# Optimization experiments

Measured on AMD Instinct MI355X. Metric: run time of the kernel, lower is better.

The kernel has to match this reference:

```python
import jax, jax.numpy as jnp
import numpy as np

MASK = 1
PAD = 0
N_ITER = 3
B, N, D, VOCAB = 8, 1024, 256, 32000
PAD_START = 960  # positions >= PAD_START are PAD tokens


def make_positional(d, max_len):
    pos = jnp.arange(max_len, dtype=jnp.float32)[:, None]          # [L,1]
    di = jnp.arange(d // 2, dtype=jnp.float32) / (d // 2)          # [d/2]
    ang = (10000.0 ** (-di))[None, :] * pos                        # [L,d/2]
    return jnp.concatenate([jnp.sin(ang), jnp.cos(ang)], axis=-1)  # [L,d]


def setup_inputs() -> dict:
    rng = np.random.default_rng(0)
    ix = rng.integers(2, VOCAB, size=(B, N), dtype=np.int64)
    ix[:, PAD_START:] = PAD
    pos = np.arange(PAD_START)
    mpos = pos[pos % 15 == 7]                      # 64 masked positions per row
    ix[:, mpos] = MASK
    mask_idx = (np.arange(B)[:, None] * N + mpos[None, :]).reshape(-1).astype(np.int32)  # [512]

    key = jax.random.key(0)
    k1, k2, k3, k4 = jax.random.split(key, 4)
    emb = jax.random.normal(k1, (VOCAB, D), dtype=jnp.float32) * 0.02
    Wq = jax.random.normal(k2, (D, D), dtype=jnp.float32) * 0.02
    Wk = jax.random.normal(k3, (D, D), dtype=jnp.float32) * 0.02
    Wv = jax.random.normal(k4, (D, D), dtype=jnp.float32) * 0.02
    return {"ix": jnp.asarray(ix), "mask_idx": jnp.asarray(mask_idx),
            "emb": emb, "Wq": Wq, "Wk": Wk, "Wv": Wv}


def reference(ix, mask_idx, emb, Wq, Wk, Wv):
    d = emb.shape[1]
    n = ix.shape[-1]
    sqd = np.sqrt(d).astype(np.float32)
    PE = make_positional(d, n)                                  # [n,d]

    mask = (ix == MASK)[..., None]                              # [B,n,1] bool
    pad = (ix == PAD)[..., None].astype(jnp.float32)            # [B,n,1]
    padm = (pad + jnp.swapaxes(pad, -2, -1)) > 0                # [B,n,n] bool
    mask_inf = jnp.where(padm, -9999.0, 0.0).astype(jnp.float32)

    X = jnp.where(mask, 0.0, emb[ix])                           # [B,n,d]
    Q = jnp.zeros((X.shape[0], n, d), jnp.float32)
    K = jnp.zeros_like(Q)
    V = jnp.zeros_like(Q)
    H = jnp.zeros_like(Q)
    S = jnp.zeros((X.shape[0], n, n), jnp.float32)

    def update_S(Q, K, H, V):
        scores = (jnp.einsum('bnd,bmd->bnm', Q, K)
                  + jnp.einsum('bnd,bmd->bnm', H, V) + mask_inf) / sqd
        Sn = jax.nn.softmax(scores, axis=-1)
        return jnp.where(padm, 0.0, Sn)

    logits = None
    for _ in range(N_ITER):
        Xp = X + PE[None]                                       # [B,n,d]
        Q = Xp @ Wq.T + S @ K
        K = Xp @ Wk.T + jnp.einsum('bmn,bmd->bnd', S, Q)        # S^T @ Q
        V = Xp @ Wv.T + jnp.einsum('bmn,bmd->bnd', S, H)        # S^T @ H
        S = update_S(Q, K, H, V)
        H = S @ V
        S = update_S(Q, K, H, V)
        V = Xp @ Wv.T + jnp.einsum('bmn,bmd->bnd', S, H)
        K = Xp @ Wk.T + jnp.einsum('bmn,bmd->bnd', S, Q)
        Q = Xp @ Wq.T + S @ K
        Xm = V @ Wv + K @ Wk + Q @ Wq                           # [B,n,d] (note: no transpose, as in torch)
        X = jnp.where(mask, Xm, X)
        Xm_rows = Xm.reshape(-1, d)[mask_idx]                   # [n_masked, d]
        logits = Xm_rows @ emb.T                                # [n_masked, vocab]
    return logits
```

## Files before the change

### kernel.cpp

```cpp
#include <hip/hip_runtime.h>
#include <hip/hip_bf16.h>
#include <hip/hip_fp16.h>

typedef __attribute__((ext_vector_type(8))) short bf16x8;
typedef __attribute__((ext_vector_type(4))) float f32x4;
typedef unsigned short u16;

static __device__ __forceinline__ u16 f2bf(float f) {
    union { float f; unsigned int i; } c; c.f = f;
    unsigned int r = c.i + 0x7fffu + ((c.i >> 16) & 1u);
    return (u16)(r >> 16);
}
static __device__ __forceinline__ u16 f2h(float f) {
    __half h = __float2half(f);
    return *(u16*)&h;
}
static __device__ __forceinline__ float h2f(u16 u) {
    __half h = *(__half*)&u;
    return __half2float(h);
}

#define AS1(p) ((const __attribute__((address_space(1))) void*)(p))
#define AS3(p) ((__attribute__((address_space(3))) void*)(p))
static __device__ __forceinline__ void glds16(const void* g, void* l) {
    __builtin_amdgcn_global_load_lds(AS1(g), AS3(l), 16, 0, 0);
}

static __device__ __forceinline__ void xcdmap(int nwg, int nx, int& x, int& y, int& z) {
    const int lin = blockIdx.x;
    const int per = nwg >> 3;
    const int swz = (lin & 7) * per + (lin >> 3);
    z = swz / per;
    const int rem = swz - z * per;
    x = rem % nx;
    y = rem / nx;
}

static constexpr long B_EMB  = 0;
static constexpr long B_SF   = 16777216;
static constexpr long B_SXP  = B_SF   + 33554432;
static constexpr long B_STXP = B_SXP  + 20971520;
static constexpr long B_QH   = B_STXP + 20971520;
static constexpr long B_KVQ  = B_QH   + 8388608;
static constexpr long B_BQ   = B_KVQ  + 12582912;
static constexpr long B_BKV  = B_BQ   + 5242880;
static constexpr long B_VT   = B_BKV  + 10485760;
static constexpr long B_W3T  = B_VT   + 4194304;
static constexpr long B_XRB  = B_W3T  + 393216;
static constexpr long B_PE   = B_XRB  + 262144;
static constexpr long B_PAD  = B_PE   + 1048576;
static constexpr long B_MSK  = B_PAD  + 32768;

static constexpr long sSX  = 1024L * 1280;
static constexpr long sQH  = 1024L * 512;
static constexpr long sKVQ = 1024L * 768;
static constexpr long sBQ  = 256L * 1280;
static constexpr long sBKV = 512L * 1280;
static constexpr long sVT  = 256L * 1024;
static constexpr long sS2  = 1024L * 1024;

__global__ __launch_bounds__(256) void k_setup(float* __restrict__ PE, const int* __restrict__ ix,
                                               int* __restrict__ padf, int* __restrict__ maskf,
                                               const float* __restrict__ Wq, const float* __restrict__ Wk,
                                               const float* __restrict__ Wv, const float* __restrict__ emb,
                                               char* __restrict__ base) {
    __shared__ u16 tile[32][33];
    const int bid = blockIdx.x;
    if (bid < 512) {
        int g = bid * 256 + threadIdx.x;
        int p = g >> 7, j = g & 127;
        float di   = (float)j * (1.0f / 128.0f);
        float freq = powf(10000.0f, -di);
        float ang  = (float)p * freq;
        PE[(long)p * 256 + j]       = sinf(ang);
        PE[(long)p * 256 + j + 128] = cosf(ang);
        return;
    }
    if (bid < 544) {
        int g = (bid - 512) * 256 + threadIdx.x;
        int tok = ix[g];
        padf[g]  = (tok == 0) ? 1 : 0;
        maskf[g] = (tok == 1) ? 1 : 0;
        return;
    }
    if (bid < 2080) {
        const int idx = bid - 544;
        const int bz = idx >> 6, rem = idx & 63;
        const int bx = rem >> 3, by = rem & 7;
        const int ws = bz >> 3, rb8 = bz & 7;
        const float* W; u16 *rep, *T; long repStride;
        if (ws == 0)      { W = Wk; rep = (u16*)(base + B_BKV);               T = (u16*)(base + B_W3T);       repStride = sBKV; }
        else if (ws == 1) { W = Wv; rep = (u16*)(base + B_BKV) + 256L * 1280; T = (u16*)(base + B_W3T) + 256; repStride = sBKV; }
        else              { W = Wq; rep = (u16*)(base + B_BQ);                T = (u16*)(base + B_W3T) + 512; repStride = sBQ; }
        rep += (long)rb8 * repStride;
        const int tx = threadIdx.x & 31, ty = threadIdx.x >> 5;
#pragma unroll
        for (int rr = 0; rr < 32; rr += 8) {
            int r = bx * 32 + ty + rr, c = by * 32 + tx;
            u16 u = f2bf(W[(long)r * 256 + c]);
            rep[(long)r * 1280 + c] = u;
            if (rb8 == 0) tile[ty + rr][tx] = u;
        }
        if (rb8 == 0) {
            __syncthreads();
#pragma unroll
            for (int rr = 0; rr < 32; rr += 8)
                T[(long)(by * 32 + ty + rr) * 768 + bx * 32 + tx] = tile[tx][ty + rr];
        }
        return;
    }
    long e = ((long)(bid - 2080) * 256 + threadIdx.x) * 4;
    float4 v = *(const float4*)(emb + e);
    ushort4 o;
    o.x = f2bf(v.x); o.y = f2bf(v.y); o.z = f2bf(v.z); o.w = f2bf(v.w);
    *(ushort4*)((u16*)(base + B_EMB) + e) = o;
}

__global__ __launch_bounds__(256) void k_embx(const int* __restrict__ ix, const float* __restrict__ emb,
                                              const float* __restrict__ PE,
                                              u16* __restrict__ SXp, u16* __restrict__ STXp) {
    int g = blockIdx.x * 256 + threadIdx.x;
    long e = (long)g * 4;
    long bn = e >> 8;
    int i = (int)(bn & 1023), c = (int)(e & 255);
    int tok = ix[bn];
    float4 v;
    if (tok == 1) v = make_float4(0.f, 0.f, 0.f, 0.f);
    else          v = *(const float4*)(emb + (long)tok * 256 + c);
    float4 p = *(const float4*)(PE + (long)i * 256 + c);
    ushort4 o;
    o.x = f2bf(v.x + p.x); o.y = f2bf(v.y + p.y);
    o.z = f2bf(v.z + p.z); o.w = f2bf(v.w + p.w);
    long oo = bn * 1280 + c;
    *(ushort4*)(SXp + oo)  = o;
    *(ushort4*)(STXp + oo) = o;
}

__global__ __launch_bounds__(256)
void k_gupd(const u16* __restrict__ SXp, const u16* __restrict__ STXp,
            u16* __restrict__ BQ, u16* __restrict__ BKV,
            u16* __restrict__ QHb, u16* __restrict__ KVQ, u16* __restrict__ VTb, int K) {
    int xb, y, z;
    xcdmap(768, 8, xb, y, z);
    const int i0 = xb * 128;
    const u16 *A, *B;
    u16 *outR, *outR2, *T;
    int j0, ldR, ldT, jloc;
    if (y < 4) {
        j0 = y << 6;
        A = SXp + (long)z * sSX;  B = BQ + (long)z * sBQ;
        outR  = QHb + (long)z * sQH;          ldR = 512;
        outR2 = KVQ + 512 + (long)z * sKVQ;
        T = BKV + 256 + (long)z * sBKV;       ldT = 1280; jloc = j0;
    } else {
        j0 = (y - 4) << 6;
        A = STXp + (long)z * sSX;  B = BKV + (long)z * sBKV;
        outR  = KVQ + (long)z * sKVQ;         ldR = 768;
        outR2 = nullptr;
        if (j0 < 256) { T = BQ + 256 + (long)z * sBQ; ldT = 1280; jloc = j0; }
        else          { T = VTb + (long)z * sVT;      ldT = 1024; jloc = j0 - 256; }
    }

    __shared__ u16 As[128 * 32];
    __shared__ u16 Bs[64 * 32];
    __shared__ u16 Tt[64][136];
    const int t = threadIdx.x, w = t >> 6, l = t & 63;
    const int wr = (w >> 1) << 6, wc = (w & 1) << 5;
    const int lr = l & 15, lk = (l >> 4) << 3;
    f32x4 acc[4][2] = {};

    const u16* ga = A + (long)(i0 + (t >> 2)) * 1280 + ((t & 3) << 3);
    const u16* gb = B + (long)(j0 + (t >> 2)) * 1280 + ((t & 3) << 3);
    const long a64 = 1280L << 6;
    char* lA = (char*)As + (w << 10);
    char* lB = (char*)Bs + (w << 10);

    for (int k0 = 0; k0 < K; k0 += 32) {
        glds16(ga + k0,       lA);
        glds16(ga + k0 + a64, lA + 4096);
        glds16(gb + k0,       lB);
        __syncthreads();
        bf16x8 af[4], bb[2];
#pragma unroll
        for (int m = 0; m < 4; ++m)
            af[m] = *(const bf16x8*)(As + ((wr + (m << 4) + lr) << 5) + lk);
#pragma unroll
        for (int n = 0; n < 2; ++n)
            bb[n] = *(const bf16x8*)(Bs + ((wc + (n << 4) + lr) << 5) + lk);
#pragma unroll
        for (int m = 0; m < 4; ++m)
#pragma unroll
            for (int n = 0; n < 2; ++n)
                acc[m][n] = __builtin_amdgcn_mfma_f32_16x16x32_bf16(af[m], bb[n], acc[m][n], 0, 0, 0);
        __syncthreads();
    }

    const int rb  = wr + ((l >> 4) << 2);
    const int cbl = wc + lr;
#pragma unroll
    for (int m = 0; m < 4; ++m)
#pragma unroll
        for (int n = 0; n < 2; ++n)
#pragma unroll
            for (int j = 0; j < 4; ++j) {
                u16 u = f2bf(acc[m][n][j]);
                int rl = rb + (m << 4) + j;
                int cl = cbl + (n << 4);
                outR[(long)(i0 + rl) * ldR + j0 + cl] = u;
                if (outR2) outR2[(long)(i0 + rl) * 768 + j0 + cl] = u;
                Tt[cl][rl] = u;
            }
    __syncthreads();
#pragma unroll
    for (int p = 0; p < 4; ++p) {
        int id = p * 256 + t;
        int jj = id >> 4, ch = id & 15;
        uint4 v = *(const uint4*)&Tt[jj][ch << 3];
        *(uint4*)(T + (long)(jloc + jj) * ldT + i0 + (ch << 3)) = v;
    }
}

__global__ __launch_bounds__(256)
void k_gbf(int nwg, int ny,
           const u16* __restrict__ A, int lda, long sA, int K,
           const u16* __restrict__ B, int ldb, long sB,
           u16* __restrict__ outR, int ldR, long sR,
           u16* __restrict__ outR2, int ldR2, long sR2,
           u16* __restrict__ outT1, int ldT1, long sT1,
           u16* __restrict__ outT2, int ldT2, long sT2, int jSplit) {
    int xb, yb, z;
    xcdmap(nwg, 8, xb, yb, z);
    (void)ny;
    A    += (long)z * sA;
    B    += (long)z * sB;
    outR += (long)z * sR;
    if (outR2) outR2 += (long)z * sR2;
    const int i0 = xb * 128, j0 = yb * 64;
    u16* T; int ldT; long sT; int jloc;
    if (j0 < jSplit) { T = outT1; ldT = ldT1; sT = sT1; jloc = j0; }
    else             { T = outT2; ldT = ldT2; sT = sT2; jloc = j0 - jSplit; }
    T += (long)z * sT;

    __shared__ u16 As[128 * 32];
    __shared__ u16 Bs[64 * 32];
    __shared__ u16 Tt[64][136];
    const int t = threadIdx.x, w = t >> 6, l = t & 63;
    const int wr = (w >> 1) << 6, wc = (w & 1) << 5;
    const int lr = l & 15, lk = (l >> 4) << 3;
    f32x4 acc[4][2] = {};

    const u16* ga = A + (long)(i0 + (t >> 2)) * lda + ((t & 3) << 3);
    const u16* gb = B + (long)(j0 + (t >> 2)) * ldb + ((t & 3) << 3);
    const long a64 = (long)lda << 6;
    char* lA = (char*)As + (w << 10);
    char* lB = (char*)Bs + (w << 10);

    for (int k0 = 0; k0 < K; k0 += 32) {
        glds16(ga + k0,       lA);
        glds16(ga + k0 + a64, lA + 4096);
        glds16(gb + k0,       lB);
        __syncthreads();
        bf16x8 af[4], bb[2];
#pragma unroll
        for (int m = 0; m < 4; ++m)
            af[m] = *(const bf16x8*)(As + ((wr + (m << 4) + lr) << 5) + lk);
#pragma unroll
        for (int n = 0; n < 2; ++n)
            bb[n] = *(const bf16x8*)(Bs + ((wc + (n << 4) + lr) << 5) + lk);
#pragma unroll
        for (int m = 0; m < 4; ++m)
#pragma unroll
            for (int n = 0; n < 2; ++n)
                acc[m][n] = __builtin_amdgcn_mfma_f32_16x16x32_bf16(af[m], bb[n], acc[m][n], 0, 0, 0);
        __syncthreads();
    }

    const int rb  = wr + ((l >> 4) << 2);
    const int cbl = wc + lr;
#pragma unroll
    for (int m = 0; m < 4; ++m)
#pragma unroll
        for (int n = 0; n < 2; ++n)
#pragma unroll
            for (int j = 0; j < 4; ++j) {
                u16 u = f2bf(acc[m][n][j]);
                int rl = rb + (m << 4) + j;
                int cl = cbl + (n << 4);
                outR[(long)(i0 + rl) * ldR + j0 + cl] = u;
                if (outR2) outR2[(long)(i0 + rl) * ldR2 + j0 + cl] = u;
                Tt[cl][rl] = u;
            }
    __syncthreads();
#pragma unroll
    for (int p = 0; p < 4; ++p) {
        int id = p * 256 + t;
        int jj = id >> 4, ch = id & 15;
        uint4 v = *(const uint4*)&Tt[jj][ch << 3];
        *(uint4*)(T + (long)(jloc + jj) * ldT + i0 + (ch << 3)) = v;
    }
}

__global__ __launch_bounds__(256)
void k_mf(const u16* __restrict__ A, const u16* __restrict__ B, u16* __restrict__ C,
          int K, int lda, int ldb, int ldc, long sA, long sB, long sC) {
    int xb, yb, z;
    xcdmap(512, 8, xb, yb, z);
    A += (long)z * sA;
    B += (long)z * sB;
    C += (long)z * sC;
    const int i0 = xb * 128, j0 = yb * 128;
    __shared__ u16 As[128 * 32];
    __shared__ u16 Bs[128 * 32];
    const int t = threadIdx.x, w = t >> 6, l = t & 63;
    const int wr = (w >> 1) << 6, wc = (w & 1) << 6;
    const int lr = l & 15, lk = (l >> 4) << 3;
    f32x4 acc[4][4] = {};
    const u16* ga = A + (long)(i0 + (t >> 2)) * lda + ((t & 3) << 3);
    const u16* gb = B + (long)(j0 + (t >> 2)) * ldb + ((t & 3) << 3);
    const long a64 = (long)lda << 6, b64 = (long)ldb << 6;
    char* lA = (char*)As + (w << 10);
    char* lB = (char*)Bs + (w << 10);
    for (int k0 = 0; k0 < K; k0 += 32) {
        glds16(ga + k0,       lA);
        glds16(ga + k0 + a64, lA + 4096);
        glds16(gb + k0,       lB);
        glds16(gb + k0 + b64, lB + 4096);
        __syncthreads();
        bf16x8 af[4], bfr[4];
#pragma unroll
        for (int m = 0; m < 4; ++m)
            af[m] = *(const bf16x8*)(As + ((wr + (m << 4) + lr) << 5) + lk);
#pragma unroll
        for (int n = 0; n < 4; ++n)
            bfr[n] = *(const bf16x8*)(Bs + ((wc + (n << 4) + lr) << 5) + lk);
#pragma unroll
        for (int m = 0; m < 4; ++m)
#pragma unroll
            for (int n = 0; n < 4; ++n)
                acc[m][n] = __builtin_amdgcn_mfma_f32_16x16x32_bf16(af[m], bfr[n], acc[m][n], 0, 0, 0);
        __syncthreads();
    }
    const int rb = i0 + wr + ((l >> 4) << 2);
    const int cb = j0 + wc + lr;
#pragma unroll
    for (int m = 0; m < 4; ++m)
#pragma unroll
        for (int n = 0; n < 4; ++n)
#pragma unroll
            for (int j = 0; j < 4; ++j)
                C[(long)(rb + (m << 4) + j) * ldc + cb + (n << 4)] = f2h(acc[m][n][j]);
}

__global__ __launch_bounds__(256)
void k_smtr(const u16* __restrict__ Sf, u16* __restrict__ SXp, u16* __restrict__ STXp,
            const int* __restrict__ padf) {
    int bx, yb, b;
    xcdmap(1024, 128, bx, yb, b);
    (void)yb;
    const int t = threadIdx.x;
    const int r = t >> 5, cg = t & 31;
    __shared__ u16   T8[8][1028];
    __shared__ float padd[1024];
    const int r0 = bx * 8;
    const int row = r0 + r;
    const int* pr = padf + b * 1024;
#pragma unroll
    for (int k = 0; k < 4; ++k)
        padd[t * 4 + k] = pr[t * 4 + k] ? -9999.0f : 0.0f;
    __syncthreads();
    const float prow = pr[row] ? -9999.0f : 0.0f;
    const u16* src = Sf + ((long)(b * 1024 + row)) * 1024;

    float e[32];
    float m = -3.0e38f;
#pragma unroll
    for (int q = 0; q < 8; ++q) {
        int c = cg * 4 + q * 128;
        ushort4 v = *(const ushort4*)(src + c);
#pragma unroll
        for (int j = 0; j < 4; ++j) {
            float x = (h2f((&v.x)[j]) + fminf(prow, padd[c + j])) * 0.0625f;
            e[q * 4 + j] = x;
            m = fmaxf(m, x);
        }
    }
#pragma unroll
    for (int o = 1; o < 32; o <<= 1) m = fmaxf(m, __shfl_xor(m, o));

    float s = 0.f;
#pragma unroll
    for (int i = 0; i < 32; ++i) { e[i] = expf(e[i] - m); s += e[i]; }
#pragma unroll
    for (int o = 1; o < 32; o <<= 1) s += __shfl_xor(s, o);
    const float inv = 1.0f / s;

    u16* orow = SXp + ((long)(b * 1024 + row)) * 1280 + 256;
#pragma unroll
    for (int q = 0; q < 8; ++q) {
        int c = cg * 4 + q * 128;
        ushort4 o4;
#pragma unroll
        for (int j = 0; j < 4; ++j)
            (&o4.x)[j] = (fminf(prow, padd[c + j]) < 0.f) ? (u16)0 : f2bf(e[q * 4 + j] * inv);
        *(ushort4*)(orow + c) = o4;
        *(ushort4*)&T8[r][c] = o4;
    }
    __syncthreads();
#pragma unroll
    for (int p = 0; p < 4; ++p) {
        int c = t + p * 256;
        u16 tmp[8];
#pragma unroll
        for (int rr = 0; rr < 8; ++rr) tmp[rr] = T8[rr][c];
        *(uint4*)(STXp + ((long)(b * 1024 + c)) * 1280 + 256 + r0) = *(uint4*)&tmp[0];
    }
}

__global__ __launch_bounds__(256)
void k_xmr(const u16* __restrict__ KVQ, const u16* __restrict__ W3T,
           const int* __restrict__ midx, const float* __restrict__ PE,
           u16* __restrict__ SXp, u16* __restrict__ STXp, u16* __restrict__ XRb, int last) {
    const int i0 = blockIdx.x * 128, j0 = blockIdx.y * 64;
    __shared__ u16 As[128 * 32];
    __shared__ u16 Bs[64 * 32];
    const int t = threadIdx.x, w = t >> 6, l = t & 63;
    const int wr = (w >> 1) << 6, wc = (w & 1) << 5;
    const int lr = l & 15, lk = (l >> 4) << 3;
    f32x4 acc[4][2] = {};
    const int r1 = i0 + (t >> 2);
    const u16* ga1 = KVQ + (long)midx[r1]      * 768 + ((t & 3) << 3);
    const u16* ga2 = KVQ + (long)midx[r1 + 64] * 768 + ((t & 3) << 3);
    const u16* gb  = W3T + (long)(j0 + (t >> 2)) * 768 + ((t & 3) << 3);
    char* lA = (char*)As + (w << 10);
    char* lB = (char*)Bs + (w << 10);
    for (int k0 = 0; k0 < 768; k0 += 32) {
        glds16(ga1 + k0, lA);
        glds16(ga2 + k0, lA + 4096);
        glds16(gb  + k0, lB);
        __syncthreads();
        bf16x8 af[4], bb[2];
#pragma unroll
        for (int m = 0; m < 4; ++m)
            af[m] = *(const bf16x8*)(As + ((wr + (m << 4) + lr) << 5) + lk);
#pragma unroll
        for (int n = 0; n < 2; ++n)
            bb[n] = *(const bf16x8*)(Bs + ((wc + (n << 4) + lr) << 5) + lk);
#pragma unroll
        for (int m = 0; m < 4; ++m)
#pragma unroll
            for (int n = 0; n < 2; ++n)
                acc[m][n] = __builtin_amdgcn_mfma_f32_16x16x32_bf16(af[m], bb[n], acc[m][n], 0, 0, 0);
        __syncthreads();
    }
    const int rb = wr + ((l >> 4) << 2);
    const int cb = wc + lr;
#pragma unroll
    for (int m = 0; m < 4; ++m)
#pragma unroll
        for (int n = 0; n < 2; ++n)
#pragma unroll
            for (int j = 0; j < 4; ++j) {
                int row = i0 + rb + (m << 4) + j;
                int col = j0 + cb + (n << 4);
                if (last) {
                    XRb[(long)row * 256 + col] = f2bf(acc[m][n][j]);
                } else {
                    int gr  = midx[row];
                    u16 xp = f2bf(acc[m][n][j] + PE[(long)(gr & 1023) * 256 + col]);
                    long oo = (long)gr * 1280 + col;
                    SXp[oo] = xp; STXp[oo] = xp;
                }
            }
}

__global__ __launch_bounds__(256)
void k_mfl(const u16* __restrict__ XRb, const u16* __restrict__ embB, float* __restrict__ C) {
    const int bid = blockIdx.x;
    const int by = bid % 500, bx = bid / 500;
    const int i0 = bx * 128, j0 = by * 64;
    __shared__ u16 As[128 * 32];
    __shared__ u16 Bs[64 * 32];
    const int t = threadIdx.x, w = t >> 6, l = t & 63;
    const int wr = (w >> 1) << 6, wc = (w & 1) << 5;
    const int lr = l & 15, lk = (l >> 4) << 3;
    f32x4 acc[4][2] = {};
    const u16* ga = XRb  + (long)(i0 + (t >> 2)) * 256 + ((t & 3) << 3);
    const u16* gb = embB + (long)(j0 + (t >> 2)) * 256 + ((t & 3) << 3);
    char* lA = (char*)As + (w << 10);
    char* lB = (char*)Bs + (w << 10);
    for (int k0 = 0; k0 < 256; k0 += 32) {
        glds16(ga + k0,            lA);
        glds16(ga + k0 + 64 * 256, lA + 4096);
        glds16(gb + k0,            lB);
        __syncthreads();
        bf16x8 af[4], bb[2];
#pragma unroll
        for (int m = 0; m < 4; ++m)
            af[m] = *(const bf16x8*)(As + ((wr + (m << 4) + lr) << 5) + lk);
#pragma unroll
        for (int n = 0; n < 2; ++n)
            bb[n] = *(const bf16x8*)(Bs + ((wc + (n << 4) + lr) << 5) + lk);
#pragma unroll
        for (int m = 0; m < 4; ++m)
#pragma unroll
            for (int n = 0; n < 2; ++n)
                acc[m][n] = __builtin_amdgcn_mfma_f32_16x16x32_bf16(af[m], bb[n], acc[m][n], 0, 0, 0);
        __syncthreads();
    }
    const int rb = i0 + wr + ((l >> 4) << 2);
    const int cb = j0 + wc + lr;
#pragma unroll
    for (int m = 0; m < 4; ++m)
#pragma unroll
        for (int n = 0; n < 2; ++n)
#pragma unroll
            for (int j = 0; j < 4; ++j)
                C[(long)(rb + (m << 4) + j) * 32000 + cb + (n << 4)] = acc[m][n][j];
}

extern "C" void kernel_launch(void* const* d_in, const int* in_sizes, int n_in,
                              void* d_out, int out_size, void* d_ws, size_t ws_size,
                              hipStream_t stream) {
    (void)in_sizes; (void)n_in; (void)out_size; (void)ws_size;
    const int*   ix   = (const int*)d_in[0];
    const int*   midx = (const int*)d_in[1];
    const float* emb  = (const float*)d_in[2];
    const float* Wq   = (const float*)d_in[3];
    const float* Wk   = (const float*)d_in[4];
    const float* Wv   = (const float*)d_in[5];

    char* base = (char*)d_ws;
    u16*   embB = (u16*)(base + B_EMB);
    u16*   Sf   = (u16*)(base + B_SF);
    u16*   SXp  = (u16*)(base + B_SXP);
    u16*   STXp = (u16*)(base + B_STXP);
    u16*   QHb  = (u16*)(base + B_QH);
    u16*   KVQ  = (u16*)(base + B_KVQ);
    u16*   BQ   = (u16*)(base + B_BQ);
    u16*   BKV  = (u16*)(base + B_BKV);
    u16*   VTb  = (u16*)(base + B_VT);
    u16*   W3T  = (u16*)(base + B_W3T);
    u16*   XRb  = (u16*)(base + B_XRB);
    float* PEf  = (float*)(base + B_PE);
    int*   padf  = (int*)(base + B_PAD);
    int*   maskf = (int*)(base + B_MSK);
    float* out  = (float*)d_out;

    k_setup<<<10080, 256, 0, stream>>>(PEf, ix, padf, maskf, Wq, Wk, Wv, emb, base);
    k_embx <<<2048, 256, 0, stream>>>(ix, emb, PEf, SXp, STXp);

    const int JBIG = 1 << 30;

    for (int it = 0; it < 3; ++it) {
        const int KU = it ? 1216 : 256;
        k_gupd<<<768, 256, 0, stream>>>(SXp, STXp, BQ, BKV, QHb, KVQ, VTb, KU);
        k_mf<<<512, 256, 0, stream>>>(QHb, KVQ, Sf, it ? 512 : 256, 512, 768, 1024, sQH, sKVQ, sS2);
        k_smtr<<<1024, 256, 0, stream>>>(Sf, SXp, STXp, padf);
        k_gbf<<<256, 256, 0, stream>>>(256, 4,
                                       SXp + 256, 1280, sSX, 960, VTb, 1024, sVT,
                                       QHb + 256, 512, sQH, nullptr, 0, 0,
                                       BKV + 256L * 1280 + 256, 1280, sBKV,
                                       BKV + 256L * 1280 + 256, 1280, sBKV, JBIG);
        k_mf<<<512, 256, 0, stream>>>(QHb, KVQ, Sf, 512, 512, 768, 1024, sQH, sKVQ, sS2);
        k_smtr<<<1024, 256, 0, stream>>>(Sf, SXp, STXp, padf);
        k_gbf<<<512, 256, 0, stream>>>(512, 8,
                                       STXp, 1280, sSX, 1216, BKV, 1280, sBKV,
                                       KVQ, 768, sKVQ, nullptr, 0, 0,
                                       BQ + 256, 1280, sBQ, VTb, 1024, sVT, 256);
        k_gbf<<<256, 256, 0, stream>>>(256, 4,
                                       SXp, 1280, sSX, 1216, BQ, 1280, sBQ,
                                       QHb, 512, sQH, KVQ + 512, 768, sKVQ,
                                       BKV + 256, 1280, sBKV, BKV + 256, 1280, sBKV, JBIG);
        k_xmr<<<dim3(4, 4, 1), 256, 0, stream>>>(KVQ, W3T, midx, PEf, SXp, STXp, XRb,
                                                 (it == 2) ? 1 : 0);
    }
    k_mfl<<<2000, 256, 0, stream>>>(XRb, embB, out);
}
```

Measured before the change: 568.2 us.

## Update second score matrix incrementally from H delta instead of full recompute

The second score computation is replaced by an incremental update. The H GEMM kernel now stores the difference between the new and old H, and a new rank-256 kernel adds dH·V^T into the existing fp16 pre-softmax score buffer rather than recomputing Q·K^T + H·V^T over K=512. This halves the K dimension of that score GEMM but adds a read-modify-write of the 1024x1024 score matrix per batch, plus an extra DH buffer write. It relies on the raw scores in Sf being kept unmodified by k_smtr, and the bf16/fp16 rounding of the delta and accumulator may drift numerically.

```diff
diff --git a/kernel.cpp b/kernel.cpp
--- a/kernel.cpp
+++ b/kernel.cpp
@@ -10,6 +10,9 @@
     union { float f; unsigned int i; } c; c.f = f;
     unsigned int r = c.i + 0x7fffu + ((c.i >> 16) & 1u);
     return (u16)(r >> 16);
+}
+static __device__ __forceinline__ float bf2f(u16 u) {
+    union { unsigned int i; float f; } c; c.i = ((unsigned int)u) << 16; return c.f;
 }
 static __device__ __forceinline__ u16 f2h(float f) {
     __half h = __float2half(f);
@@ -50,6 +53,7 @@
 static constexpr long B_PE   = B_XRB  + 262144;
 static constexpr long B_PAD  = B_PE   + 1048576;
 static constexpr long B_MSK  = B_PAD  + 32768;
+static constexpr long B_DH   = B_MSK  + 32768;
 
 static constexpr long sSX  = 1024L * 1280;
 static constexpr long sQH  = 1024L * 512;
@@ -58,6 +62,7 @@
 static constexpr long sBKV = 512L * 1280;
 static constexpr long sVT  = 256L * 1024;
 static constexpr long sS2  = 1024L * 1024;
+static constexpr long sDH  = 1024L * 256;
 
 __global__ __launch_bounds__(256) void k_setup(float* __restrict__ PE, const int* __restrict__ ix,
                                                int* __restrict__ padf, int* __restrict__ maskf,
@@ -144,19 +149,17 @@
     xcdmap(768, 8, xb, y, z);
     const int i0 = xb * 128;
     const u16 *A, *B;
-    u16 *outR, *outR2, *T;
+    u16 *outR, *T;
     int j0, ldR, ldT, jloc;
     if (y < 4) {
         j0 = y << 6;
         A = SXp + (long)z * sSX;  B = BQ + (long)z * sBQ;
         outR  = QHb + (long)z * sQH;          ldR = 512;
-        outR2 = KVQ + 512 + (long)z * sKVQ;
         T = BKV + 256 + (long)z * sBKV;       ldT = 1280; jloc = j0;
     } else {
         j0 = (y - 4) << 6;
         A = STXp + (long)z * sSX;  B = BKV + (long)z * sBKV;
         outR  = KVQ + (long)z * sKVQ;         ldR = 768;
-        outR2 = nullptr;
         if (j0 < 256) { T = BQ + 256 + (long)z * sBQ; ldT = 1280; jloc = j0; }
         else          { T = VTb + (long)z * sVT;      ldT = 1024; jloc = j0 - 256; }
     }
@@ -207,7 +210,6 @@
                 int rl = rb + (m << 4) + j;
                 int cl = cbl + (n << 4);
                 outR[(long)(i0 + rl) * ldR + j0 + cl] = u;
-                if (outR2) outR2[(long)(i0 + rl) * 768 + j0 + cl] = u;
                 Tt[cl][rl] = u;
             }
     __syncthreads();
@@ -217,6 +219,80 @@
         int jj = id >> 4, ch = id & 15;
         uint4 v = *(const uint4*)&Tt[jj][ch << 3];
         *(uint4*)(T + (long)(jloc + jj) * ldT + i0 + (ch << 3)) = v;
+    }
+}
+
+__global__ __launch_bounds__(256)
+void k_gbh(const u16* __restrict__ SXp, const u16* __restrict__ VTb,
+           u16* __restrict__ QHb, u16* __restrict__ BKV, u16* __restrict__ DH, int it0) {
+    int xb, yb, z;
+    xcdmap(256, 8, xb, yb, z);
+    const u16* A = SXp + 256 + (long)z * sSX;
+    const u16* B = VTb + (long)z * sVT;
+    u16* outR = QHb + 256 + (long)z * sQH;
+    u16* T    = BKV + 256L * 1280 + 256 + (long)z * sBKV;
+    u16* dh   = DH + (long)z * sDH;
+    const int i0 = xb * 128, j0 = yb * 64;
+
+    __shared__ u16 As[128 * 32];
+    __shared__ u16 Bs[64 * 32];
+    __shared__ u16 Tt[64][136];
+    const int t = threadIdx.x, w = t >> 6, l = t & 63;
+    const int wr = (w >> 1) << 6, wc = (w & 1) << 5;
+    const int lr = l & 15, lk = (l >> 4) << 3;
+    f32x4 acc[4][2] = {};
+
+    const u16* ga = A + (long)(i0 + (t >> 2)) * 1280 + ((t & 3) << 3);
+    const u16* gb = B + (long)(j0 + (t >> 2)) * 1024 + ((t & 3) << 3);
+    const long a64 = 1280L << 6;
+    char* lA = (char*)As + (w << 10);
+    char* lB = (char*)Bs + (w << 10);
+
+    for (int k0 = 0; k0 < 960; k0 += 32) {
+        glds16(ga + k0,       lA);
+        glds16(ga + k0 + a64, lA + 4096);
+        glds16(gb + k0,       lB);
+        __syncthreads();
+        bf16x8 af[4], bb[2];
+#pragma unroll
+        for (int m = 0; m < 4; ++m)
+            af[m] = *(const bf16x8*)(As + ((wr + (m << 4) + lr) << 5) + lk);
+#pragma unroll
+        for (int n = 0; n < 2; ++n)
+            bb[n] = *(const bf16x8*)(Bs + ((wc + (n << 4) + lr) << 5) + lk);
+#pragma unroll
+        for (int m = 0; m < 4; ++m)
+#pragma unroll
+            for (int n = 0; n < 2; ++n)
+                acc[m][n] = __builtin_amdgcn_mfma_f32_16x16x32_bf16(af[m], bb[n], acc[m][n], 0, 0, 0);
+        __syncthreads();
+    }
+
+    const int rb  = wr + ((l >> 4) << 2);
+    const int cbl = wc + lr;
+#pragma unroll
+    for (int m = 0; m < 4; ++m)
+#pragma unroll
+        for (int n = 0; n < 2; ++n)
+#pragma unroll
+            for (int j = 0; j < 4; ++j) {
+                u16 hn = f2bf(acc[m][n][j]);
+                int rl = rb + (m << 4) + j;
+                int cl = cbl + (n << 4);
+                long ro = (long)(i0 + rl) * 512 + j0 + cl;
+                float dv = bf2f(hn);
+                if (!it0) dv -= bf2f(outR[ro]);
+                outR[ro] = hn;
+                dh[(long)(i0 + rl) * 256 + j0 + cl] = f2bf(dv);
+                Tt[cl][rl] = hn;
+            }
+    __syncthreads();
+#pragma unroll
+    for (int p = 0; p < 4; ++p) {
+        int id = p * 256 + t;
+        int jj = id >> 4, ch = id & 15;
+        uint4 v = *(const uint4*)&Tt[jj][ch << 3];
+        *(uint4*)(T + (long)(jj + j0) * 1280 + i0 + (ch << 3)) = v;
     }
 }
 
@@ -352,6 +428,58 @@
 }
 
 __global__ __launch_bounds__(256)
+void k_mfa(const u16* __restrict__ DH, const u16* __restrict__ KVQ, u16* __restrict__ C) {
+    int xb, yb, z;
+    xcdmap(512, 8, xb, yb, z);
+    const u16* A = DH + (long)z * sDH;
+    const u16* B = KVQ + 256 + (long)z * sKVQ;
+    u16* Cc = C + (long)z * sS2;
+    const int i0 = xb * 128, j0 = yb * 128;
+    __shared__ u16 As[128 * 32];
+    __shared__ u16 Bs[128 * 32];
+    const int t = threadIdx.x, w = t >> 6, l = t & 63;
+    const int wr = (w >> 1) << 6, wc = (w & 1) << 6;
+    const int lr = l & 15, lk = (l >> 4) << 3;
+    f32x4 acc[4][4] = {};
+    const u16* ga = A + (long)(i0 + (t >> 2)) * 256 + ((t & 3) << 3);
+    const u16* gb = B + (long)(j0 + (t >> 2)) * 768 + ((t & 3) << 3);
+    const long a64 = 256L << 6, b64 = 768L << 6;
+    char* lA = (char*)As + (w << 10);
+    char* lB = (char*)Bs + (w << 10);
+    for (int k0 = 0; k0 < 256; k0 += 32) {
+        glds16(ga + k0,       lA);
+        glds16(ga + k0 + a64, lA + 4096);
+        glds16(gb + k0,       lB);
+        glds16(gb + k0 + b64, lB + 4096);
+        __syncthreads();
+        bf16x8 af[4], bfr[4];
+#pragma unroll
+        for (int m = 0; m < 4; ++m)
+            af[m] = *(const bf16x8*)(As + ((wr + (m << 4) + lr) << 5) + lk);
+#pragma unroll
+        for (int n = 0; n < 4; ++n)
+            bfr[n] = *(const bf16x8*)(Bs + ((wc + (n << 4) + lr) << 5) + lk);
+#pragma unroll
+        for (int m = 0; m < 4; ++m)
+#pragma unroll
+            for (int n = 0; n < 4; ++n)
+                acc[m][n] = __builtin_amdgcn_mfma_f32_16x16x32_bf16(af[m], bfr[n], acc[m][n], 0, 0, 0);
+        __syncthreads();
+    }
+    const int rb = i0 + wr + ((l >> 4) << 2);
+    const int cb = j0 + wc + lr;
+#pragma unroll
+    for (int m = 0; m < 4; ++m)
+#pragma unroll
+        for (int n = 0; n < 4; ++n)
+#pragma unroll
+            for (int j = 0; j < 4; ++j) {
+                long off = (long)(rb + (m << 4) + j) * 1024 + cb + (n << 4);
+                Cc[off] = f2h(h2f(Cc[off]) + acc[m][n][j]);
+            }
+}
+
+__global__ __launch_bounds__(256)
 void k_smtr(const u16* __restrict__ Sf, u16* __restrict__ SXp, u16* __restrict__ STXp,
             const int* __restrict__ padf) {
     int bx, yb, b;
@@ -544,6 +672,7 @@
     float* PEf  = (float*)(base + B_PE);
     int*   padf  = (int*)(base + B_PAD);
     int*   maskf = (int*)(base + B_MSK);
+    u16*   DH   = (u16*)(base + B_DH);
     float* out  = (float*)d_out;
 
     k_setup<<<10080, 256, 0, stream>>>(PEf, ix, padf, maskf, Wq, Wk, Wv, emb, base);
@@ -556,12 +685,8 @@
         k_gupd<<<768, 256, 0, stream>>>(SXp, STXp, BQ, BKV, QHb, KVQ, VTb, KU);
         k_mf<<<512, 256, 0, stream>>>(QHb, KVQ, Sf, it ? 512 : 256, 512, 768, 1024, sQH, sKVQ, sS2);
         k_smtr<<<1024, 256, 0, stream>>>(Sf, SXp, STXp, padf);
-        k_gbf<<<256, 256, 0, stream>>>(256, 4,
-                                       SXp + 256, 1280, sSX, 960, VTb, 1024, sVT,
-                                       QHb + 256, 512, sQH, nullptr, 0, 0,
-                                       BKV + 256L * 1280 + 256, 1280, sBKV,
-                                       BKV + 256L * 1280 + 256, 1280, sBKV, JBIG);
-        k_mf<<<512, 256, 0, stream>>>(QHb, KVQ, Sf, 512, 512, 768, 1024, sQH, sKVQ, sS2);
+        k_gbh<<<256, 256, 0, stream>>>(SXp, VTb, QHb, BKV, DH, (it == 0) ? 1 : 0);
+        k_mfa<<<512, 256, 0, stream>>>(DH, KVQ, Sf);
         k_smtr<<<1024, 256, 0, stream>>>(Sf, SXp, STXp, padf);
         k_gbf<<<512, 256, 0, stream>>>(512, 8,
                                        STXp, 1280, sSX, 1216, BKV, 1280, sBKV,
```

New measurement: 560.1 us. Within noise of the previous version (-1.4%).
